# Performance work log

Measured on AMD Instinct MI355X. Metric: run time of the kernel, lower is better.

Reference implementation:

```python
import jax, jax.numpy as jnp
import numpy as np

N, NCLS, D = 512, 100000, 128
SCALE, MARGIN = 64.0, 0.5
EPS_BN = 1e-5
EPS_NORM = 1e-12


def _init_conv(key, shape):
    # Kaiming-ish init for conv weights (OIHW)
    fan_in = float(np.prod(shape[1:]))
    return jax.random.normal(key, shape, jnp.float32) * np.float32(np.sqrt(2.0 / fan_in))


def setup_inputs() -> dict:
    key = jax.random.key(0)
    ks = jax.random.split(key, 8)
    return {
        "x": jax.random.normal(ks[0], (N, 1, 112, 112), jnp.float32),
        "gt": jax.random.randint(ks[1], (N,), 0, NCLS, dtype=jnp.int32),
        "w1": _init_conv(ks[2], (16, 1, 4, 4)),  "b1": jnp.zeros(16),  "g1": jnp.ones(16),  "be1": jnp.zeros(16),
        "w2": _init_conv(ks[3], (32, 16, 4, 4)), "b2": jnp.zeros(32),  "g2": jnp.ones(32),  "be2": jnp.zeros(32),
        "w3": _init_conv(ks[4], (64, 32, 3, 3)), "b3": jnp.zeros(64),  "g3": jnp.ones(64),  "be3": jnp.zeros(64),
        "w4": _init_conv(ks[5], (128, 64, 3, 3)),"b4": jnp.zeros(128), "g4": jnp.ones(128), "be4": jnp.zeros(128),
        # xavier-uniform ArcFace weight (out_size, in_size)
        "arc_w": jax.random.uniform(ks[6], (NCLS, D), jnp.float32, -1.0, 1.0) * np.float32(np.sqrt(6.0 / (NCLS + D))),
    }


def _conv_bn_relu(x, w, b, g, be, stride, pad):
    y = jax.lax.conv_general_dilated(
        x, w, (stride, stride), [(pad, pad), (pad, pad)],
        dimension_numbers=("NCHW", "OIHW", "NCHW"))
    y = y + b[None, :, None, None]
    # BatchNorm in training mode: batch statistics, biased variance
    mu = y.mean((0, 2, 3), keepdims=True)
    var = ((y - mu) ** 2).mean((0, 2, 3), keepdims=True)
    yn = (y - mu) * jax.lax.rsqrt(var + EPS_BN)
    return jax.nn.relu(yn * g[None, :, None, None] + be[None, :, None, None])


def _l2norm(v):
    return v / jnp.maximum(jnp.linalg.norm(v, axis=1, keepdims=True), EPS_NORM)


def reference(x, gt, w1, b1, g1, be1, w2, b2, g2, be2, w3, b3, g3, be3,
              w4, b4, g4, be4, arc_w):
    h = _conv_bn_relu(x, w1, b1, g1, be1, stride=2, pad=1)   # (N,16,56,56)
    h = _conv_bn_relu(h, w2, b2, g2, be2, stride=2, pad=1)   # (N,32,28,28)
    h = _conv_bn_relu(h, w3, b3, g3, be3, stride=1, pad=0)   # (N,64,26,26)
    h = _conv_bn_relu(h, w4, b4, g4, be4, stride=1, pad=0)   # (N,128,24,24)
    f = h.mean((2, 3))                                        # global avg pool -> (N,128)

    logit = _l2norm(f) @ _l2norm(arc_w).T                     # (N, NCLS) cosine logits
    n = logit.shape[0]
    rows = jnp.arange(n)
    orig = logit[rows, gt]                                    # target cosines
    marg = jnp.cos(jnp.arccos(orig) + MARGIN)                 # cos(theta + m)
    out = logit.at[rows, gt].add(marg - orig)                 # scatter margin correction
    return SCALE * out
```

## Files before the change

### kernel.cpp

```cpp
#include <hip/hip_runtime.h>

typedef unsigned int uint;
typedef unsigned short ushort;

typedef _Float16 half8 __attribute__((ext_vector_type(8)));
typedef float f32x4 __attribute__((ext_vector_type(4)));

#define DEV __device__ __forceinline__

DEV ushort f2h(float x) {
    _Float16 h = (_Float16)x;
    ushort u;
    __builtin_memcpy(&u, &h, 2);
    return u;
}

__global__ __launch_bounds__(256, 2) void conv1_k(
    const float* __restrict__ x, const float* __restrict__ w,
    const float* __restrict__ bias, ushort* __restrict__ y1,
    float* __restrict__ sums)
{
    int idx = blockIdx.x * 256 + threadIdx.x;
    int ow = idx % 56;
    int oh = (idx / 56) % 56;
    int n  = idx / 3136;

    float acc[16];
#pragma unroll
    for (int o = 0; o < 16; ++o) acc[o] = bias[o];

    const float* xp = x + (size_t)n * 12544;
#pragma unroll
    for (int kh = 0; kh < 4; ++kh) {
        int ih = oh * 2 - 1 + kh;
        if ((uint)ih >= 112u) continue;
#pragma unroll
        for (int kw = 0; kw < 4; ++kw) {
            int iw = ow * 2 - 1 + kw;
            if ((uint)iw >= 112u) continue;
            float v = xp[ih * 112 + iw];
#pragma unroll
            for (int o = 0; o < 16; ++o)
                acc[o] = fmaf(v, w[o * 16 + kh * 4 + kw], acc[o]);
        }
    }

    ushort hs[16];
#pragma unroll
    for (int o = 0; o < 16; ++o) hs[o] = f2h(acc[o]);
    __builtin_memcpy(y1 + (size_t)idx * 16, hs, 32);

    __shared__ float red[2][4][16];
    int lane = threadIdx.x & 63, wv = threadIdx.x >> 6;
#pragma unroll
    for (int o = 0; o < 16; ++o) {
        float s = acc[o], q = acc[o] * acc[o];
#pragma unroll
        for (int off = 32; off; off >>= 1) {
            s += __shfl_down(s, off);
            q += __shfl_down(q, off);
        }
        if (lane == 0) { red[0][wv][o] = s; red[1][wv][o] = q; }
    }
    __syncthreads();
    float* sl = sums + (blockIdx.x & 7) * 256;
    int t = threadIdx.x;
    if (t < 16)
        atomicAdd(&sl[t], red[0][0][t] + red[0][1][t] + red[0][2][t] + red[0][3][t]);
    else if (t >= 64 && t < 80) {
        int o = t - 64;
        atomicAdd(&sl[128 + o], red[1][0][o] + red[1][1][o] + red[1][2][o] + red[1][3][o]);
    }
}

__global__ __launch_bounds__(128) void mkab(const float* __restrict__ sums,
                                            const float* __restrict__ g,
                                            const float* __restrict__ be,
                                            float* __restrict__ ab, int C, float invP)
{
    int c = threadIdx.x;
    if (c >= C) return;
    float s = 0.f, q = 0.f;
#pragma unroll
    for (int k = 0; k < 8; ++k) { s += sums[k * 256 + c]; q += sums[k * 256 + 128 + c]; }
    float mu  = s * invP;
    float var = fmaf(-mu, mu, q * invP);
    float a   = g[c] / sqrtf(var + 1e-5f);
    ab[c]     = a;
    ab[C + c] = fmaf(-mu, a, be[c]);
}

template <int C>
__global__ __launch_bounds__(256) void fold(const ushort* __restrict__ y,
                                            const float* __restrict__ ab,
                                            ushort* __restrict__ h)
{
    __shared__ float sa[C], sb[C];
    if (threadIdx.x < C) { sa[threadIdx.x] = ab[threadIdx.x]; sb[threadIdx.x] = ab[C + threadIdx.x]; }
    __syncthreads();
    int idx = blockIdx.x * 256 + threadIdx.x;
    half8 v;
    __builtin_memcpy(&v, y + (size_t)idx * 8, 16);
    int c0 = (idx * 8) & (C - 1);
    half8 o;
#pragma unroll
    for (int e = 0; e < 8; ++e) {
        float f = (float)v[e];
        o[e] = (_Float16)fmaxf(fmaf(sa[c0 + e], f, sb[c0 + e]), 0.f);
    }
    __builtin_memcpy(h + (size_t)idx * 8, &o, 16);
}

template <int OC, int IC, int K>
__global__ __launch_bounds__(256) void repack(const float* __restrict__ w,
                                              ushort* __restrict__ wb)
{
    int i = blockIdx.x * 256 + threadIdx.x;
    int ic = i % IC;
    int r  = i / IC;
    int kw = r % K;  r /= K;
    int kh = r % K;
    int oc = r / K;
    wb[i] = f2h(w[((oc * IC + ic) * K + kh) * K + kw]);
}

template <int OC, int IC, int K>
__global__ __launch_bounds__(256) void repack_cm(const float* __restrict__ w,
                                                 ushort* __restrict__ wb)
{
    constexpr int NC = IC / 32;
    int i = blockIdx.x * 256 + threadIdx.x;
    int e  = i & 31;
    int oc = (i >> 5) % OC;
    int q  = i / (32 * OC);
    int c  = q % NC;
    int r  = q / NC;
    int kw = r % K, kh = r / K;
    int ic = c * 32 + e;
    wb[i] = f2h(w[((oc * IC + ic) * K + kh) * K + kw]);
}

__global__ __launch_bounds__(256, 2) void conv2_mfma(
    const ushort* __restrict__ hin, const ushort* __restrict__ wb,
    const float* __restrict__ bias, ushort* __restrict__ y,
    float* __restrict__ sums)
{
    const int lane = threadIdx.x & 63, wv = threadIdx.x >> 6;
    const int col = lane & 15, quad = lane >> 4;
    const int kwoff = quad >> 1;
    const int icoff = (quad & 1) * 8;
    const int mbase = blockIdx.x * 128 + wv * 32;

    int nb[2], ihb[2], iwb[2];
#pragma unroll
    for (int s = 0; s < 2; ++s) {
        int m = mbase + s * 16 + col;
        int n = m / 784, rem = m % 784;
        int oh = rem / 28, ow = rem % 28;
        nb[s]  = n * 50176 + icoff;
        ihb[s] = oh * 2 - 1;
        iwb[s] = ow * 2 - 1 + kwoff;
    }

    float bv[2];
#pragma unroll
    for (int t = 0; t < 2; ++t) bv[t] = bias[t * 16 + col];

    f32x4 acc[2][2];
#pragma unroll
    for (int s = 0; s < 2; ++s)
#pragma unroll
        for (int t = 0; t < 2; ++t) acc[s][t] = (f32x4){0.f, 0.f, 0.f, 0.f};

    const int wrow = col * 256 + icoff;

#pragma unroll
    for (int kh = 0; kh < 4; ++kh) {
#pragma unroll
        for (int kwp = 0; kwp < 2; ++kwp) {
            half8 af[2];
#pragma unroll
            for (int s = 0; s < 2; ++s) {
                int ih = ihb[s] + kh;
                int iw = iwb[s] + kwp * 2;
                uint r0 = 0, r1 = 0, r2 = 0, r3 = 0;
                if ((uint)ih < 56u && (uint)iw < 56u) {
                    uint raw[4];
                    __builtin_memcpy(raw, hin + nb[s] + ih * 896 + iw * 16, 16);
                    r0 = raw[0]; r1 = raw[1]; r2 = raw[2]; r3 = raw[3];
                }
                uint raw2[4] = {r0, r1, r2, r3};
                __builtin_memcpy(&af[s], raw2, 16);
            }
            const int boff = (kh * 4 + kwp * 2 + kwoff) * 16;
#pragma unroll
            for (int t = 0; t < 2; ++t) {
                half8 bf;
                __builtin_memcpy(&bf, wb + wrow + t * 4096 + boff, 16);
#pragma unroll
                for (int s = 0; s < 2; ++s)
                    acc[s][t] = __builtin_amdgcn_mfma_f32_16x16x32_f16(af[s], bf, acc[s][t], 0, 0, 0);
            }
        }
    }

    float ss[2] = {0.f, 0.f}, qq[2] = {0.f, 0.f};
#pragma unroll
    for (int s = 0; s < 2; ++s) {
        int m0 = mbase + s * 16 + quad * 4;
#pragma unroll
        for (int t = 0; t < 2; ++t) {
#pragma unroll
            for (int r = 0; r < 4; ++r) {
                float yv = acc[s][t][r] + bv[t];
                ss[t] += yv;
                qq[t] = fmaf(yv, yv, qq[t]);
                y[(size_t)(m0 + r) * 32 + t * 16 + col] = f2h(yv);
            }
        }
    }
    __shared__ float redS[4][32], redQ[4][32];
#pragma unroll
    for (int t = 0; t < 2; ++t) {
        float s = ss[t], q = qq[t];
        s += __shfl_xor(s, 16); s += __shfl_xor(s, 32);
        q += __shfl_xor(q, 16); q += __shfl_xor(q, 32);
        if (quad == 0) { redS[wv][t * 16 + col] = s; redQ[wv][t * 16 + col] = q; }
    }
    __syncthreads();
    int t0 = threadIdx.x;
    float* sl = sums + (blockIdx.x & 7) * 256;
    if (t0 < 32)
        atomicAdd(&sl[t0], redS[0][t0] + redS[1][t0] + redS[2][t0] + redS[3][t0]);
    else if (t0 >= 128 && t0 < 160) {
        int c = t0 - 128;
        atomicAdd(&sl[128 + c], redQ[0][c] + redQ[1][c] + redQ[2][c] + redQ[3][c]);
    }
}

template <int IC, int OC, int K, int IH, int IW, int OH, int OW>
__global__ __launch_bounds__(256, 2) void conv_lds(
    const ushort* __restrict__ hin, const ushort* __restrict__ wb,
    const float* __restrict__ bias, ushort* __restrict__ y,
    float* __restrict__ sums)
{
    constexpr int NT  = OC / 16, NC = IC / 32;
    constexpr int NCH = K * K * NC;
    constexpr int ROWB = IW * IC * 2;
    constexpr int MAXR = 255 / OW + K;
    constexpr int SLAB = ((MAXR * ROWB + 4095) / 4096) * 4096;
    __shared__ ushort slab[SLAB / 2];
    __shared__ float redS[4][OC], redQ[4][OC];

    const int lane = threadIdx.x & 63, wv = threadIdx.x >> 6;
    const int col = lane & 15, quad = lane >> 4;
    const int mbase = blockIdx.x * 256 + wv * 64;

    const int m0  = blockIdx.x * 256;
    const int rl0 = (m0 / (OH * OW)) * IH + (m0 % (OH * OW)) / OW;
    const int mL  = m0 + 255;
    const int rl1 = (mL / (OH * OW)) * IH + (mL % (OH * OW)) / OW + (K - 1);
    const int stage_bytes = (rl1 - rl0 + 1) * ROWB;

    {
        const char* src = (const char*)(hin + (size_t)rl0 * (IW * IC));
        char* dst = (char*)slab;
        int d = threadIdx.x * 16;
        int rounds = (stage_bytes + 4095) >> 12;
        for (int r = 0; r < rounds; ++r) {
            int sw = d ^ (((d >> 7) & 7) << 4);
            __builtin_amdgcn_global_load_lds(
                (const __attribute__((address_space(1))) void*)(src + sw),
                (__attribute__((address_space(3))) void*)(dst + d), 16, 0, 0);
            d += 4096;
        }
    }

    int aloc[4];
#pragma unroll
    for (int s = 0; s < 4; ++s) {
        int m = mbase + s * 16 + col;
        int n = m / (OH * OW), rem = m % (OH * OW);
        int oh = rem / OW, ow = rem % OW;
        aloc[s] = ((n * IH + oh - rl0) * IW + ow) * IC + quad * 8;
    }
    const int bcol = col * 32 + quad * 8;

    f32x4 acc[4][NT];
#pragma unroll
    for (int s = 0; s < 4; ++s)
#pragma unroll
        for (int t = 0; t < NT; ++t) acc[s][t] = (f32x4){0.f, 0.f, 0.f, 0.f};

    half8 bbuf[2][NT];
#pragma unroll
    for (int t = 0; t < NT; ++t)
        __builtin_memcpy(&bbuf[0][t], wb + t * 512 + bcol, 16);

    __syncthreads();

#pragma unroll
    for (int q = 0; q < NCH; ++q) {
        if (q + 1 < NCH) {
            const ushort* bp = wb + (q + 1) * (OC * 32) + bcol;
#pragma unroll
            for (int t = 0; t < NT; ++t)
                __builtin_memcpy(&bbuf[(q + 1) & 1][t], bp + t * 512, 16);
        }
        const int kh = q / (K * NC), kw = (q / NC) % K, c = q % NC;
        const int aoff = (kh * IW + kw) * IC + c * 32;
#pragma unroll
        for (int s = 0; s < 4; ++s) {
            half8 af;
            int b = 2 * (aloc[s] + aoff);
            b ^= ((b >> 7) & 7) << 4;
            __builtin_memcpy(&af, (const char*)slab + b, 16);
#pragma unroll
            for (int t = 0; t < NT; ++t)
                acc[s][t] = __builtin_amdgcn_mfma_f32_16x16x32_f16(af, bbuf[q & 1][t], acc[s][t], 0, 0, 0);
        }
    }

    float bv[NT];
#pragma unroll
    for (int t = 0; t < NT; ++t) bv[t] = bias[t * 16 + col];

    float ss[NT], qq[NT];
#pragma unroll
    for (int t = 0; t < NT; ++t) { ss[t] = 0.f; qq[t] = 0.f; }
#pragma unroll
    for (int s = 0; s < 4; ++s) {
        int me = mbase + s * 16 + quad * 4;
#pragma unroll
        for (int t = 0; t < NT; ++t) {
#pragma unroll
            for (int r = 0; r < 4; ++r) {
                float yv = acc[s][t][r] + bv[t];
                ss[t] += yv;
                qq[t] = fmaf(yv, yv, qq[t]);
                y[(size_t)(me + r) * OC + t * 16 + col] = f2h(yv);
            }
        }
    }
#pragma unroll
    for (int t = 0; t < NT; ++t) {
        float s = ss[t], q = qq[t];
        s += __shfl_xor(s, 16); s += __shfl_xor(s, 32);
        q += __shfl_xor(q, 16); q += __shfl_xor(q, 32);
        if (quad == 0) { redS[wv][t * 16 + col] = s; redQ[wv][t * 16 + col] = q; }
    }
    __syncthreads();
    int t0 = threadIdx.x;
    float* sl = sums + (blockIdx.x & 7) * 256;
    if (t0 < OC)
        atomicAdd(&sl[t0], redS[0][t0] + redS[1][t0] + redS[2][t0] + redS[3][t0]);
    else if (t0 >= 128 && t0 < 128 + OC) {
        int c = t0 - 128;
        atomicAdd(&sl[128 + c], redQ[0][c] + redQ[1][c] + redQ[2][c] + redQ[3][c]);
    }
}

__global__ __launch_bounds__(256) void pool(const ushort* __restrict__ y4,
                                            const float* __restrict__ ab,
                                            float* __restrict__ f)
{
    int n = blockIdx.x;
    int c = threadIdx.x & 127, ph = threadIdx.x >> 7;
    const ushort* p = y4 + (size_t)n * 73728 + c;
    float a = ab[c], b = ab[128 + c];
    float s = 0.f;
    for (int i = ph * 288; i < ph * 288 + 288; ++i) {
        _Float16 hv;
        __builtin_memcpy(&hv, p + i * 128, 2);
        s += fmaxf(fmaf(a, (float)hv, b), 0.f);
    }
    __shared__ float l[128];
    if (ph == 1) l[c] = s;
    __syncthreads();
    if (ph == 0) f[n * 128 + c] = (s + l[c]) * (1.f / 576.f);
}

__global__ __launch_bounds__(128) void fnorm(const float* __restrict__ f,
                                             ushort* __restrict__ fnh)
{
    int n = blockIdx.x, t = threadIdx.x;
    float v = f[n * 128 + t];
    float q = v * v;
    for (int off = 32; off; off >>= 1) q += __shfl_down(q, off);
    __shared__ float l[2];
    if ((t & 63) == 0) l[t >> 6] = q;
    __syncthreads();
    float inv = 1.f / fmaxf(sqrtf(l[0] + l[1]), 1e-12f);
    fnh[n * 128 + t] = f2h(v * inv);
}

__global__ __launch_bounds__(256) void wnorm(const float* __restrict__ w,
                                             float* __restrict__ winv)
{
    int wv = threadIdx.x >> 6, lane = threadIdx.x & 63;
    int j = blockIdx.x * 4 + wv;
    const float* p = w + (size_t)j * 128;
    float v0 = p[lane], v1 = p[lane + 64];
    float q = fmaf(v0, v0, v1 * v1);
    for (int off = 32; off; off >>= 1) q += __shfl_down(q, off);
    if (lane == 0) winv[j] = 1.f / fmaxf(sqrtf(q), 1e-12f);
}

__global__ __launch_bounds__(256) void arc_gemm(const ushort* __restrict__ fnh,
                                                const float* __restrict__ aw,
                                                const float* __restrict__ winv,
                                                const int* __restrict__ gt,
                                                float* __restrict__ out)
{
    const int lane = threadIdx.x & 63, wv = threadIdx.x >> 6;
    const int col = lane & 15, quad = lane >> 4;
    const int j = blockIdx.x * 64 + wv * 16 + col;
    const bool jvalid = (j < 100000);
    const int jc = jvalid ? j : 99999;

    const float wi = winv[jc];
    const float* wp = aw + (size_t)jc * 128 + quad * 8;
    half8 bfr[4];
#pragma unroll
    for (int s = 0; s < 4; ++s) {
        half8 t;
#pragma unroll
        for (int e = 0; e < 8; ++e) t[e] = (_Float16)(wp[s * 32 + e] * wi);
        bfr[s] = t;
    }

    const float cm = 0.87758256189037272f;
    const float sm = 0.47942553860420301f;

    for (int mt = 0; mt < 32; ++mt) {
        const ushort* ap = fnh + (size_t)(mt * 16 + col) * 128 + quad * 8;
        f32x4 acc = {0.f, 0.f, 0.f, 0.f};
#pragma unroll
        for (int s = 0; s < 4; ++s) {
            half8 af;
            __builtin_memcpy(&af, ap + s * 32, 16);
            acc = __builtin_amdgcn_mfma_f32_16x16x32_f16(af, bfr[s], acc, 0, 0, 0);
        }
#pragma unroll
        for (int r = 0; r < 4; ++r) {
            int row = mt * 16 + quad * 4 + r;
            float v = acc[r];
            float o = 64.f * v;
            if (gt[row] == j) {
                float t = fmaxf(1.f - v * v, 0.f);
                o = 64.f * fmaf(v, cm, -sqrtf(t) * sm);
            }
            if (jvalid) out[(size_t)row * 100000 + j] = o;
        }
    }
}

extern "C" void kernel_launch(void* const* d_in, const int* in_sizes, int n_in,
                              void* d_out, int out_size, void* d_ws, size_t ws_size,
                              hipStream_t stream)
{
    const float* x   = (const float*)d_in[0];
    const int*   gt  = (const int*)d_in[1];
    const float* w1  = (const float*)d_in[2];
    const float* b1  = (const float*)d_in[3];
    const float* g1  = (const float*)d_in[4];
    const float* be1 = (const float*)d_in[5];
    const float* w2  = (const float*)d_in[6];
    const float* b2  = (const float*)d_in[7];
    const float* g2  = (const float*)d_in[8];
    const float* be2 = (const float*)d_in[9];
    const float* w3  = (const float*)d_in[10];
    const float* b3  = (const float*)d_in[11];
    const float* g3  = (const float*)d_in[12];
    const float* be3 = (const float*)d_in[13];
    const float* w4  = (const float*)d_in[14];
    const float* b4  = (const float*)d_in[15];
    const float* g4  = (const float*)d_in[16];
    const float* be4 = (const float*)d_in[17];
    const float* aw  = (const float*)d_in[18];
    float* out = (float*)d_out;

    float* ws = (float*)d_ws;
    ushort* yb  = (ushort*)ws;
    ushort* hb  = (ushort*)(ws + 18874368);
    ushort* wb2 = (ushort*)(ws + 31719424);
    ushort* wb3 = (ushort*)(ws + 31723520);
    ushort* wb4 = (ushort*)(ws + 31732736);
    float* sums = ws + 31769600;
    float* ab   = ws + 31777792;
    float* fbuf = ws + 31778816;
    ushort* fnh = (ushort*)(ws + 31844352);
    float* wiv  = ws + 31877120;

    hipMemsetAsync(sums, 0, 4 * 2048 * sizeof(float), stream);

    repack<32, 16, 4><<<32, 256, 0, stream>>>(w2, wb2);
    repack_cm<64, 32, 3><<<72, 256, 0, stream>>>(w3, wb3);
    repack_cm<128, 64, 3><<<288, 256, 0, stream>>>(w4, wb4);
    wnorm<<<25000, 256, 0, stream>>>(aw, wiv);

    conv1_k<<<6272, 256, 0, stream>>>(x, w1, b1, yb, sums);
    mkab<<<1, 128, 0, stream>>>(sums, g1, be1, ab, 16, 1.f / 1605632.f);
    fold<16><<<12544, 256, 0, stream>>>(yb, ab, hb);

    conv2_mfma<<<3136, 256, 0, stream>>>(hb, wb2, b2, yb, sums + 2048);
    mkab<<<1, 128, 0, stream>>>(sums + 2048, g2, be2, ab + 256, 32, 1.f / 401408.f);
    fold<32><<<6272, 256, 0, stream>>>(yb, ab + 256, hb);

    conv_lds<32, 64, 3, 28, 28, 26, 26><<<1352, 256, 0, stream>>>(hb, wb3, b3, yb, sums + 4096);
    mkab<<<1, 128, 0, stream>>>(sums + 4096, g3, be3, ab + 512, 64, 1.f / 346112.f);
    fold<64><<<10816, 256, 0, stream>>>(yb, ab + 512, hb);

    conv_lds<64, 128, 3, 26, 26, 24, 24><<<1152, 256, 0, stream>>>(hb, wb4, b4, yb, sums + 6144);
    mkab<<<1, 128, 0, stream>>>(sums + 6144, g4, be4, ab + 768, 128, 1.f / 294912.f);

    pool<<<512, 256, 0, stream>>>(yb, ab + 768, fbuf);
    fnorm<<<512, 128, 0, stream>>>(fbuf, fnh);

    arc_gemm<<<1563, 256, 0, stream>>>(fnh, aw, wiv, gt, out);
}
```

Baseline: 643.5 us.

## Prepack normalized fp16 ArcFace weights and emit vectorized nontemporal output stores

```diff
diff --git a/kernel.cpp b/kernel.cpp
--- a/kernel.cpp
+++ b/kernel.cpp
@@ -394,64 +394,79 @@
     fnh[n * 128 + t] = f2h(v * inv);
 }
 
-__global__ __launch_bounds__(256) void wnorm(const float* __restrict__ w,
-                                             float* __restrict__ winv)
+__global__ __launch_bounds__(256) void wpack(const float* __restrict__ w,
+                                             ushort* __restrict__ w16)
 {
     int wv = threadIdx.x >> 6, lane = threadIdx.x & 63;
     int j = blockIdx.x * 4 + wv;
     const float* p = w + (size_t)j * 128;
     float v0 = p[lane], v1 = p[lane + 64];
     float q = fmaf(v0, v0, v1 * v1);
+#pragma unroll
     for (int off = 32; off; off >>= 1) q += __shfl_down(q, off);
-    if (lane == 0) winv[j] = 1.f / fmaxf(sqrtf(q), 1e-12f);
+    float inv = 1.f / fmaxf(sqrtf(__shfl(q, 0)), 1e-12f);
+    w16[(size_t)j * 128 + lane]      = f2h(v0 * inv);
+    w16[(size_t)j * 128 + lane + 64] = f2h(v1 * inv);
 }
 
 __global__ __launch_bounds__(256) void arc_gemm(const ushort* __restrict__ fnh,
-                                                const float* __restrict__ aw,
-                                                const float* __restrict__ winv,
+                                                const ushort* __restrict__ w16,
                                                 const int* __restrict__ gt,
                                                 float* __restrict__ out)
 {
     const int lane = threadIdx.x & 63, wv = threadIdx.x >> 6;
     const int col = lane & 15, quad = lane >> 4;
-    const int j = blockIdx.x * 64 + wv * 16 + col;
-    const bool jvalid = (j < 100000);
-    const int jc = jvalid ? j : 99999;
-
-    const float wi = winv[jc];
-    const float* wp = aw + (size_t)jc * 128 + quad * 8;
+    const int jbase = blockIdx.x * 64 + wv * 16;
+    if (jbase >= 100000) return;
+
     half8 bfr[4];
-#pragma unroll
-    for (int s = 0; s < 4; ++s) {
-        half8 t;
-#pragma unroll
-        for (int e = 0; e < 8; ++e) t[e] = (_Float16)(wp[s * 32 + e] * wi);
-        bfr[s] = t;
-    }
+    const ushort* wp = w16 + (size_t)(jbase + col) * 128 + quad * 8;
+#pragma unroll
+    for (int s = 0; s < 4; ++s)
+        __builtin_memcpy(&bfr[s], wp + s * 32, 16);
 
     const float cm = 0.87758256189037272f;
     const float sm = 0.47942553860420301f;
-
-    for (int mt = 0; mt < 32; ++mt) {
-        const ushort* ap = fnh + (size_t)(mt * 16 + col) * 128 + quad * 8;
+    const int j0 = jbase + quad * 4;
+
+    half8 afA[4], afB[4];
+    const ushort* ap0 = fnh + (size_t)col * 128 + quad * 8;
+#pragma unroll
+    for (int s = 0; s < 4; ++s)
+        __builtin_memcpy(&afA[s], ap0 + s * 32, 16);
+
+    auto step = [&](int mt, half8 (&cur)[4], half8 (&nxt)[4]) {
+        if (mt + 1 < 32) {
+            const ushort* apn = fnh + (size_t)((mt + 1) * 16 + col) * 128 + quad * 8;
+#pragma unroll
+            for (int s = 0; s < 4; ++s)
+                __builtin_memcpy(&nxt[s], apn + s * 32, 16);
+        }
         f32x4 acc = {0.f, 0.f, 0.f, 0.f};
 #pragma unroll
-        for (int s = 0; s < 4; ++s) {
-            half8 af;
-            __builtin_memcpy(&af, ap + s * 32, 16);
-            acc = __builtin_amdgcn_mfma_f32_16x16x32_f16(af, bfr[s], acc, 0, 0, 0);
-        }
-#pragma unroll
-        for (int r = 0; r < 4; ++r) {
-            int row = mt * 16 + quad * 4 + r;
-            float v = acc[r];
-            float o = 64.f * v;
-            if (gt[row] == j) {
-                float t = fmaxf(1.f - v * v, 0.f);
-                o = 64.f * fmaf(v, cm, -sqrtf(t) * sm);
-            }
-            if (jvalid) out[(size_t)row * 100000 + j] = o;
-        }
+        for (int s = 0; s < 4; ++s)
+            acc = __builtin_amdgcn_mfma_f32_16x16x32_f16(bfr[s], cur[s], acc, 0, 0, 0);
+
+        const int m = mt * 16 + col;
+        const int d = gt[m] - j0;
+        if ((uint)d < 4u) {
+#pragma unroll
+            for (int r = 0; r < 4; ++r)
+                if (r == d) {
+                    float v = acc[r];
+                    float t = fmaxf(1.f - v * v, 0.f);
+                    acc[r] = fmaf(v, cm, -sqrtf(t) * sm);
+                }
+        }
+        f32x4 o4;
+#pragma unroll
+        for (int r = 0; r < 4; ++r) o4[r] = 64.f * acc[r];
+        __builtin_nontemporal_store(o4, (f32x4*)(out + (size_t)m * 100000 + j0));
+    };
+
+    for (int mt = 0; mt < 32; mt += 2) {
+        step(mt, afA, afB);
+        step(mt + 1, afB, afA);
     }
 }
 
@@ -483,6 +498,7 @@
     float* ws = (float*)d_ws;
     ushort* yb  = (ushort*)ws;
     ushort* hb  = (ushort*)(ws + 18874368);
+    ushort* w16 = hb;
     ushort* wb2 = (ushort*)(ws + 31719424);
     ushort* wb3 = (ushort*)(ws + 31723520);
     ushort* wb4 = (ushort*)(ws + 31732736);
@@ -490,14 +506,12 @@
     float* ab   = ws + 31777792;
     float* fbuf = ws + 31778816;
     ushort* fnh = (ushort*)(ws + 31844352);
-    float* wiv  = ws + 31877120;
 
     hipMemsetAsync(sums, 0, 4 * 2048 * sizeof(float), stream);
 
     repack<32, 16, 4><<<32, 256, 0, stream>>>(w2, wb2);
     repack_cm<64, 32, 3><<<72, 256, 0, stream>>>(w3, wb3);
     repack_cm<128, 64, 3><<<288, 256, 0, stream>>>(w4, wb4);
-    wnorm<<<25000, 256, 0, stream>>>(aw, wiv);
 
     conv1_k<<<6272, 256, 0, stream>>>(x, w1, b1, yb, sums);
     mkab<<<1, 128, 0, stream>>>(sums, g1, be1, ab, 16, 1.f / 1605632.f);
@@ -514,8 +528,10 @@
     conv_lds<64, 128, 3, 26, 26, 24, 24><<<1152, 256, 0, stream>>>(hb, wb4, b4, yb, sums + 6144);
     mkab<<<1, 128, 0, stream>>>(sums + 6144, g4, be4, ab + 768, 128, 1.f / 294912.f);
 
+    wpack<<<25000, 256, 0, stream>>>(aw, w16);
+
     pool<<<512, 256, 0, stream>>>(yb, ab + 768, fbuf);
     fnorm<<<512, 128, 0, stream>>>(fbuf, fnh);
 
-    arc_gemm<<<1563, 256, 0, stream>>>(fnh, aw, wiv, gt, out);
-}
+    arc_gemm<<<1563, 256, 0, stream>>>(fnh, w16, gt, out);
+}
```

Result: no change. 634.5 us (-1.4%).
